# Kernel tuning notes

Hardware: AMD Instinct MI355X
Metric: run time of the kernel (lower is better)

Reference implementation:

```python
import jax, jax.numpy as jnp
import numpy as np

TEMP = 1.0
EPS = 1e-8
NUM_SP = 2048


def setup_inputs() -> dict:
    key = jax.random.key(0)
    k1, k2, k3, k4 = jax.random.split(key, 4)
    N, C, H, W = 8, 19, 512, 512
    inputs = jax.random.normal(k1, (N, C, H, W), dtype=jnp.float32)
    # multi-hot superpixel targets in {0,1}, last column is an extra slot sliced off
    targets = jax.random.randint(k2, (N, NUM_SP, C + 1), 0, 2).astype(jnp.float32)
    superpixels = jax.random.randint(k3, (N, H, W), 0, NUM_SP, dtype=jnp.int32)
    spmasks = jax.random.bernoulli(k4, 0.5, (N, H, W))
    return {"inputs": inputs, "targets": targets,
            "superpixels": superpixels, "spmasks": spmasks}


def reference(inputs, targets, superpixels, spmasks):
    N, C, H, W = inputs.shape
    # N x HW x C, softmax over classes (permute(0,2,3,1).reshape(N,-1,C))
    logits = inputs.reshape(N, C, H * W).transpose(0, 2, 1) / TEMP
    out = jax.nn.softmax(logits, axis=2)                       # N x HW x C
    sp = superpixels.reshape(N, -1)                            # N x HW
    mask = spmasks.reshape(N, -1)                              # N x HW
    trg_sup = jax.lax.stop_gradient(targets[..., :-1])         # N x S x C (detached)
    # gather per-pixel target rows via superpixel index
    trg_pixel = jnp.take_along_axis(trg_sup, sp[:, :, None], axis=1)  # N x HW x C
    # valid = spmask AND target row non-empty
    valid = mask & jnp.any(trg_pixel != 0, axis=2)             # N x HW
    pos_pred = jnp.sum(out * trg_pixel, axis=2)                # N x HW
    loss = -jnp.sum(jnp.where(valid, jnp.log(pos_pred + EPS), 0.0))
    num_valid = 1 + jnp.sum(valid)
    return loss / num_valid
```

## Files before the change

### kernel.cpp

```cpp
#include <hip/hip_runtime.h>

#define HW_   (512 * 512)
#define NIMG  8
#define NC    19
#define NSP   2048
#define TC    20
#define NROWS (NIMG * NSP)
#define NBLK  256
#define NGRP  16
#define GSIZE (NBLK / NGRP)

typedef float vf4 __attribute__((ext_vector_type(4)));
typedef int   vi4 __attribute__((ext_vector_type(4)));


__global__ __launch_bounds__(256) void prep(
    const float* __restrict__ tgt,
    const unsigned int* __restrict__ spm,
    unsigned int* __restrict__ flag, unsigned int* __restrict__ st,
    unsigned int* __restrict__ gt, unsigned int* __restrict__ bm) {

    int gid = blockIdx.x * 256 + threadIdx.x;
    if (gid == 0) *st = 0u;
    if (gid < NGRP) gt[gid * 16] = 0u;

    if (blockIdx.x == 1 && threadIdx.x < 64) {
        unsigned int nonlow = 0, upper = 0;
        for (int i = threadIdx.x; i < 1024; i += 64) {
            unsigned int v = spm[i];
            nonlow |= (v & 0xFEFEFEFEu);
            upper  |= (v & 0xFFFFFF00u);
        }
        unsigned long long b1 = __ballot(nonlow != 0);
        unsigned long long b2 = __ballot(upper != 0);
        if (threadIdx.x == 0)
            *flag = ((b1 == 0ull) && (b2 != 0ull)) ? 0u : 1u;
    }

    const float* row = tgt + (size_t)gid * TC;
    unsigned int m = 0;
#pragma unroll
    for (int c = 0; c < NC; ++c)
        m |= (row[c] != 0.0f ? 1u : 0u) << c;
    bm[gid] = m;
}

__global__ __launch_bounds__(256, 1) void mcce_main(
    const float* __restrict__ x,
    const int*   __restrict__ sp,
    const void*  __restrict__ spm,
    const unsigned int* __restrict__ bmt,
    const unsigned int* __restrict__ flag,
    float* __restrict__ pl, unsigned int* __restrict__ pc,
    unsigned int* __restrict__ st, unsigned int* __restrict__ gt,
    float* __restrict__ out) {

    __shared__ unsigned int bmtab[NSP];
    __shared__ float sL[4];
    __shared__ unsigned int sC[4];

    int b    = blockIdx.x;
    int t    = threadIdx.x;
    int wave = t >> 6;
    int lane = t & 63;

    int n     = b & 7;
    int sbase = (b >> 3) * 8192;
    int wbase = sbase + wave * 2048;
    unsigned int flagv = *flag;

    const vi4* btv = (const vi4*)(bmt + (size_t)n * NSP);
    ((vi4*)bmtab)[t]       = btv[t];
    ((vi4*)bmtab)[t + 256] = btv[t + 256];

    const int* spw = sp + (size_t)n * HW_ + wbase;
    vi4 s4[8];
#pragma unroll
    for (int k = 0; k < 8; ++k)
        s4[k] = ((const vi4*)spw)[lane + k * 64];

    int mkb[8];
    size_t mbase = (size_t)n * HW_ + wbase;
    if (flagv) {
#pragma unroll
        for (int k = 0; k < 8; ++k) {
            vi4 m = ((const vi4*)((const int*)spm + mbase))[lane + k * 64];
            mkb[k] = (m.x != 0 ? 1 : 0) | (m.y != 0 ? 2 : 0) |
                     (m.z != 0 ? 4 : 0) | (m.w != 0 ? 8 : 0);
        }
    } else {
#pragma unroll
        for (int k = 0; k < 8; ++k) {
            unsigned int mw = ((const unsigned int*)
                               ((const unsigned char*)spm + mbase))[lane + k * 64];
            mkb[k] = ((mw        & 0xFFu) ? 1 : 0) | (((mw >> 8)  & 0xFFu) ? 2 : 0) |
                     (((mw >> 16) & 0xFFu) ? 4 : 0) | (((mw >> 24) & 0xFFu) ? 8 : 0);
        }
    }

    __syncthreads();

    unsigned int bv[8][4];
#pragma unroll
    for (int k = 0; k < 8; ++k) {
        bv[k][0] = bmtab[s4[k].x]; bv[k][1] = bmtab[s4[k].y];
        bv[k][2] = bmtab[s4[k].z]; bv[k][3] = bmtab[s4[k].w];
    }

    const float* xw = x + (size_t)n * NC * HW_ + wbase;
    vf4 A[8], B[8];
    vf4 se[8], ts[8];
#pragma unroll
    for (int k = 0; k < 8; ++k) { se[k] = (vf4){0,0,0,0}; ts[k] = (vf4){0,0,0,0}; }

#define LDC(R, c) { const vf4* p_ = (const vf4*)(xw + (size_t)(c) * HW_);      \
    _Pragma("unroll") for (int k_ = 0; k_ < 8; ++k_) R[k_] = p_[lane + k_*64]; }

#define PRC(R, c) { _Pragma("unroll") for (int k_ = 0; k_ < 8; ++k_) {         \
    vf4 e_;                                                                    \
    e_.x = __expf(R[k_].x); e_.y = __expf(R[k_].y);                            \
    e_.z = __expf(R[k_].z); e_.w = __expf(R[k_].w);                            \
    se[k_].x += e_.x; se[k_].y += e_.y; se[k_].z += e_.z; se[k_].w += e_.w;    \
    ts[k_].x += ((bv[k_][0] >> (c)) & 1) ? e_.x : 0.0f;                        \
    ts[k_].y += ((bv[k_][1] >> (c)) & 1) ? e_.y : 0.0f;                        \
    ts[k_].z += ((bv[k_][2] >> (c)) & 1) ? e_.z : 0.0f;                        \
    ts[k_].w += ((bv[k_][3] >> (c)) & 1) ? e_.w : 0.0f; } }

    LDC(A, 0)
#pragma unroll
    for (int p = 0; p < 9; ++p) {
        LDC(B, 2 * p + 1)
        PRC(A, 2 * p)
        LDC(A, 2 * p + 2)
        PRC(B, 2 * p + 1)
    }
    PRC(A, 18)

#undef LDC
#undef PRC

    float lsum = 0.0f;
    unsigned int lcnt = 0;
#pragma unroll
    for (int k = 0; k < 8; ++k) {
        if ((mkb[k] & 1) && bv[k][0]) { lsum -= __logf(ts[k].x / se[k].x + 1e-8f); ++lcnt; }
        if ((mkb[k] & 2) && bv[k][1]) { lsum -= __logf(ts[k].y / se[k].y + 1e-8f); ++lcnt; }
        if ((mkb[k] & 4) && bv[k][2]) { lsum -= __logf(ts[k].z / se[k].z + 1e-8f); ++lcnt; }
        if ((mkb[k] & 8) && bv[k][3]) { lsum -= __logf(ts[k].w / se[k].w + 1e-8f); ++lcnt; }
    }

    for (int o = 32; o > 0; o >>= 1) {
        lsum += __shfl_down(lsum, o);
        lcnt += __shfl_down(lcnt, o);
    }
    __syncthreads();
    if ((t & 63) == 0) { sL[wave] = lsum; sC[wave] = lcnt; }
    __syncthreads();

    if (t == 0) {
        float        L = sL[0] + sL[1] + sL[2] + sL[3];
        unsigned int C = sC[0] + sC[1] + sC[2] + sC[3];
        __hip_atomic_store(&pl[b], L, __ATOMIC_RELAXED, __HIP_MEMORY_SCOPE_AGENT);
        __hip_atomic_store(&pc[b], C, __ATOMIC_RELAXED, __HIP_MEMORY_SCOPE_AGENT);
        unsigned int g = (unsigned int)b / GSIZE;
        unsigned int isLast = 0u;
        unsigned int tk = __hip_atomic_fetch_add(&gt[g * 16], 1u,
                              __ATOMIC_ACQ_REL, __HIP_MEMORY_SCOPE_AGENT);
        if (tk == (unsigned int)(GSIZE - 1)) {
            unsigned int s = __hip_atomic_fetch_add(st, 1u,
                                 __ATOMIC_ACQ_REL, __HIP_MEMORY_SCOPE_AGENT);
            isLast = (s == NGRP - 1) ? 1u : 0u;
        }
        sC[0] = isLast;
    }
    __syncthreads();

    if (sC[0]) {
        float        L = 0.0f;
        unsigned int C = 0u;
        for (int i = t; i < NBLK; i += 256) {
            L += __hip_atomic_load(&pl[i], __ATOMIC_RELAXED, __HIP_MEMORY_SCOPE_AGENT);
            C += __hip_atomic_load(&pc[i], __ATOMIC_RELAXED, __HIP_MEMORY_SCOPE_AGENT);
        }
        for (int o = 32; o > 0; o >>= 1) {
            L += __shfl_down(L, o);
            C += __shfl_down(C, o);
        }
        __syncthreads();
        if ((t & 63) == 0) { sL[wave] = L; sC[wave] = C; }
        __syncthreads();
        if (t == 0) {
            L = sL[0] + sL[1] + sL[2] + sL[3];
            C = sC[0] + sC[1] + sC[2] + sC[3];
            out[0] = L / (float)(1u + C);
        }
    }
}

extern "C" void kernel_launch(void* const* d_in, const int* in_sizes, int n_in,
                              void* d_out, int out_size, void* d_ws, size_t ws_size,
                              hipStream_t stream) {
    const float* x   = (const float*)d_in[0];
    const float* tgt = (const float*)d_in[1];
    const int*   sp  = (const int*)d_in[2];
    const void*  spm = d_in[3];

    unsigned int* flag = (unsigned int*)d_ws;
    unsigned int* st   = (unsigned int*)((char*)d_ws + 4);
    unsigned int* gt   = (unsigned int*)((char*)d_ws + 64);
    float*        pl   = (float*)((char*)d_ws + 1088);
    unsigned int* pc   = (unsigned int*)((char*)d_ws + 3136);
    unsigned int* bmt  = (unsigned int*)((char*)d_ws + 5184);

    prep<<<NROWS / 256, 256, 0, stream>>>(tgt, (const unsigned int*)spm,
                                          flag, st, gt, bmt);

    mcce_main<<<NBLK, 256, 0, stream>>>(x, sp, spm, bmt, flag,
                                        pl, pc, st, gt, (float*)d_out);
}
```

Baseline: 285.2 us.

## Restructure main kernel into per-pixel-tile loop over images with asm double-buffered loads

Each block now owns a 1024-pixel tile and loops over all 8 images. Each thread loads 4 pixels across all 19 channels in one batch of inline-asm nontemporal dwordx4 loads, while the next image's batch is issued before computing the current one. The per-block LDS superpixel bitmask table is dropped in favour of direct global gathers into the bitmask array, which removes the LDS staging and one barrier. It uses far more VGPRs (two 19-vector buffers) and hand-placed vmcnt waits, which risks occupancy limits and fragile ordering.

```diff
diff --git a/kernel.cpp b/kernel.cpp
--- a/kernel.cpp
+++ b/kernel.cpp
@@ -6,6 +6,7 @@
 #define NSP   2048
 #define TC    20
 #define NROWS (NIMG * NSP)
+#define TILE  1024
 #define NBLK  256
 #define NGRP  16
 #define GSIZE (NBLK / NGRP)
@@ -55,113 +56,211 @@
     unsigned int* __restrict__ st, unsigned int* __restrict__ gt,
     float* __restrict__ out) {
 
-    __shared__ unsigned int bmtab[NSP];
     __shared__ float sL[4];
     __shared__ unsigned int sC[4];
 
     int b    = blockIdx.x;
     int t    = threadIdx.x;
     int wave = t >> 6;
-    int lane = t & 63;
-
-    int n     = b & 7;
-    int sbase = (b >> 3) * 8192;
-    int wbase = sbase + wave * 2048;
     unsigned int flagv = *flag;
 
-    const vi4* btv = (const vi4*)(bmt + (size_t)n * NSP);
-    ((vi4*)bmtab)[t]       = btv[t];
-    ((vi4*)bmtab)[t + 256] = btv[t + 256];
-
-    const int* spw = sp + (size_t)n * HW_ + wbase;
-    vi4 s4[8];
-#pragma unroll
-    for (int k = 0; k < 8; ++k)
-        s4[k] = ((const vi4*)spw)[lane + k * 64];
-
-    int mkb[8];
-    size_t mbase = (size_t)n * HW_ + wbase;
-    if (flagv) {
-#pragma unroll
-        for (int k = 0; k < 8; ++k) {
-            vi4 m = ((const vi4*)((const int*)spm + mbase))[lane + k * 64];
-            mkb[k] = (m.x != 0 ? 1 : 0) | (m.y != 0 ? 2 : 0) |
-                     (m.z != 0 ? 4 : 0) | (m.w != 0 ? 8 : 0);
-        }
-    } else {
-#pragma unroll
-        for (int k = 0; k < 8; ++k) {
-            unsigned int mw = ((const unsigned int*)
-                               ((const unsigned char*)spm + mbase))[lane + k * 64];
-            mkb[k] = ((mw        & 0xFFu) ? 1 : 0) | (((mw >> 8)  & 0xFFu) ? 2 : 0) |
-                     (((mw >> 16) & 0xFFu) ? 4 : 0) | (((mw >> 24) & 0xFFu) ? 8 : 0);
-        }
-    }
-
-    __syncthreads();
-
-    unsigned int bv[8][4];
-#pragma unroll
-    for (int k = 0; k < 8; ++k) {
-        bv[k][0] = bmtab[s4[k].x]; bv[k][1] = bmtab[s4[k].y];
-        bv[k][2] = bmtab[s4[k].z]; bv[k][3] = bmtab[s4[k].w];
-    }
-
-    const float* xw = x + (size_t)n * NC * HW_ + wbase;
-    vf4 A[8], B[8];
-    vf4 se[8], ts[8];
-#pragma unroll
-    for (int k = 0; k < 8; ++k) { se[k] = (vf4){0,0,0,0}; ts[k] = (vf4){0,0,0,0}; }
-
-#define LDC(R, c) { const vf4* p_ = (const vf4*)(xw + (size_t)(c) * HW_);      \
-    _Pragma("unroll") for (int k_ = 0; k_ < 8; ++k_) R[k_] = p_[lane + k_*64]; }
-
-#define PRC(R, c) { _Pragma("unroll") for (int k_ = 0; k_ < 8; ++k_) {         \
-    vf4 e_;                                                                    \
-    e_.x = __expf(R[k_].x); e_.y = __expf(R[k_].y);                            \
-    e_.z = __expf(R[k_].z); e_.w = __expf(R[k_].w);                            \
-    se[k_].x += e_.x; se[k_].y += e_.y; se[k_].z += e_.z; se[k_].w += e_.w;    \
-    ts[k_].x += ((bv[k_][0] >> (c)) & 1) ? e_.x : 0.0f;                        \
-    ts[k_].y += ((bv[k_][1] >> (c)) & 1) ? e_.y : 0.0f;                        \
-    ts[k_].z += ((bv[k_][2] >> (c)) & 1) ? e_.z : 0.0f;                        \
-    ts[k_].w += ((bv[k_][3] >> (c)) & 1) ? e_.w : 0.0f; } }
-
-    LDC(A, 0)
-#pragma unroll
-    for (int p = 0; p < 9; ++p) {
-        LDC(B, 2 * p + 1)
-        PRC(A, 2 * p)
-        LDC(A, 2 * p + 2)
-        PRC(B, 2 * p + 1)
-    }
-    PRC(A, 18)
-
-#undef LDC
-#undef PRC
-
+    int tpb = (b & 255) * TILE;
+    size_t thr4 = (size_t)tpb + 4 * t;
+
+    vf4 A[NC], B[NC];
+    vi4 s4A, s4B;
     float lsum = 0.0f;
     unsigned int lcnt = 0;
-#pragma unroll
-    for (int k = 0; k < 8; ++k) {
-        if ((mkb[k] & 1) && bv[k][0]) { lsum -= __logf(ts[k].x / se[k].x + 1e-8f); ++lcnt; }
-        if ((mkb[k] & 2) && bv[k][1]) { lsum -= __logf(ts[k].y / se[k].y + 1e-8f); ++lcnt; }
-        if ((mkb[k] & 4) && bv[k][2]) { lsum -= __logf(ts[k].z / se[k].z + 1e-8f); ++lcnt; }
-        if ((mkb[k] & 8) && bv[k][3]) { lsum -= __logf(ts[k].w / se[k].w + 1e-8f); ++lcnt; }
-    }
+
+#define ISSUE(S4, D, N_) do {                                                  \
+    const float* xb_  = x  + (size_t)(N_) * NC * HW_ + tpb;                    \
+    const int*   spb_ = sp + (size_t)(N_) * HW_ + tpb;                         \
+    unsigned int vo_  = (unsigned int)(t * 16);                                \
+    asm volatile(                                                              \
+        "global_load_dwordx4 %[s4],  %[vo], %[spb]\n\t"                        \
+        "global_load_dwordx4 %[d0],  %[vo], %[xb] nt\n\t"                      \
+        "v_add_u32 %[vo], 0x100000, %[vo]\n\t"                                 \
+        "global_load_dwordx4 %[d1],  %[vo], %[xb] nt\n\t"                      \
+        "v_add_u32 %[vo], 0x100000, %[vo]\n\t"                                 \
+        "global_load_dwordx4 %[d2],  %[vo], %[xb] nt\n\t"                      \
+        "v_add_u32 %[vo], 0x100000, %[vo]\n\t"                                 \
+        "global_load_dwordx4 %[d3],  %[vo], %[xb] nt\n\t"                      \
+        "v_add_u32 %[vo], 0x100000, %[vo]\n\t"                                 \
+        "global_load_dwordx4 %[d4],  %[vo], %[xb] nt\n\t"                      \
+        "v_add_u32 %[vo], 0x100000, %[vo]\n\t"                                 \
+        "global_load_dwordx4 %[d5],  %[vo], %[xb] nt\n\t"                      \
+        "v_add_u32 %[vo], 0x100000, %[vo]\n\t"                                 \
+        "global_load_dwordx4 %[d6],  %[vo], %[xb] nt\n\t"                      \
+        "v_add_u32 %[vo], 0x100000, %[vo]\n\t"                                 \
+        "global_load_dwordx4 %[d7],  %[vo], %[xb] nt\n\t"                      \
+        "v_add_u32 %[vo], 0x100000, %[vo]\n\t"                                 \
+        "global_load_dwordx4 %[d8],  %[vo], %[xb] nt\n\t"                      \
+        "v_add_u32 %[vo], 0x100000, %[vo]\n\t"                                 \
+        "global_load_dwordx4 %[d9],  %[vo], %[xb] nt\n\t"                      \
+        "v_add_u32 %[vo], 0x100000, %[vo]\n\t"                                 \
+        "global_load_dwordx4 %[d10], %[vo], %[xb] nt\n\t"                      \
+        "v_add_u32 %[vo], 0x100000, %[vo]\n\t"                                 \
+        "global_load_dwordx4 %[d11], %[vo], %[xb] nt\n\t"                      \
+        "v_add_u32 %[vo], 0x100000, %[vo]\n\t"                                 \
+        "global_load_dwordx4 %[d12], %[vo], %[xb] nt\n\t"                      \
+        "v_add_u32 %[vo], 0x100000, %[vo]\n\t"                                 \
+        "global_load_dwordx4 %[d13], %[vo], %[xb] nt\n\t"                      \
+        "v_add_u32 %[vo], 0x100000, %[vo]\n\t"                                 \
+        "global_load_dwordx4 %[d14], %[vo], %[xb] nt\n\t"                      \
+        "v_add_u32 %[vo], 0x100000, %[vo]\n\t"                                 \
+        "global_load_dwordx4 %[d15], %[vo], %[xb] nt\n\t"                      \
+        "v_add_u32 %[vo], 0x100000, %[vo]\n\t"                                 \
+        "global_load_dwordx4 %[d16], %[vo], %[xb] nt\n\t"                      \
+        "v_add_u32 %[vo], 0x100000, %[vo]\n\t"                                 \
+        "global_load_dwordx4 %[d17], %[vo], %[xb] nt\n\t"                      \
+        "v_add_u32 %[vo], 0x100000, %[vo]\n\t"                                 \
+        "global_load_dwordx4 %[d18], %[vo], %[xb] nt"                          \
+        : [d0]"=v"(D[0]),  [d1]"=v"(D[1]),  [d2]"=v"(D[2]),  [d3]"=v"(D[3]),   \
+          [d4]"=v"(D[4]),  [d5]"=v"(D[5]),  [d6]"=v"(D[6]),  [d7]"=v"(D[7]),   \
+          [d8]"=v"(D[8]),  [d9]"=v"(D[9]),  [d10]"=v"(D[10]),[d11]"=v"(D[11]), \
+          [d12]"=v"(D[12]),[d13]"=v"(D[13]),[d14]"=v"(D[14]),[d15]"=v"(D[15]), \
+          [d16]"=v"(D[16]),[d17]"=v"(D[17]),[d18]"=v"(D[18]),                  \
+          [s4]"=v"(S4), [vo]"+v"(vo_)                                          \
+        : [xb]"s"(xb_), [spb]"s"(spb_));                                       \
+} while (0)
+
+#define TIES(D) "+v"(D[0]), "+v"(D[1]), "+v"(D[2]), "+v"(D[3]), "+v"(D[4]),    \
+                "+v"(D[5]), "+v"(D[6]), "+v"(D[7]), "+v"(D[8]), "+v"(D[9]),    \
+                "+v"(D[10]), "+v"(D[11]), "+v"(D[12]), "+v"(D[13]),            \
+                "+v"(D[14]), "+v"(D[15]), "+v"(D[16]), "+v"(D[17]), "+v"(D[18])
+
+#define GATH(CS4, IT) \
+    asm volatile("s_waitcnt vmcnt(19)" : "+v"(CS4));                           \
+    __builtin_amdgcn_sched_barrier(0);                                         \
+    const unsigned int* bt_ = bmt + (IT) * NSP;                                \
+    const unsigned int* a0_ = bt_ + CS4.x;                                     \
+    const unsigned int* a1_ = bt_ + CS4.y;                                     \
+    const unsigned int* a2_ = bt_ + CS4.z;                                     \
+    const unsigned int* a3_ = bt_ + CS4.w;                                     \
+    unsigned int g0_, g1_, g2_, g3_;                                           \
+    asm volatile("global_load_dword %0, %4, off\n\t"                           \
+                 "global_load_dword %1, %5, off\n\t"                           \
+                 "global_load_dword %2, %6, off\n\t"                           \
+                 "global_load_dword %3, %7, off"                               \
+        : "=&v"(g0_), "=&v"(g1_), "=&v"(g2_), "=&v"(g3_)                       \
+        : "v"(a0_), "v"(a1_), "v"(a2_), "v"(a3_));
+
+#define COMP(CD) \
+    float se0=0, se1=0, se2=0, se3=0, ts0=0, ts1=0, ts2=0, ts3=0;              \
+    _Pragma("unroll")                                                          \
+    for (int c = 0; c < NC; ++c) {                                             \
+        float e0 = __expf(CD[c].x), e1 = __expf(CD[c].y);                      \
+        float e2 = __expf(CD[c].z), e3 = __expf(CD[c].w);                      \
+        se0 += e0; se1 += e1; se2 += e2; se3 += e3;                            \
+        ts0 += ((g0_ >> c) & 1) ? e0 : 0.0f;                                   \
+        ts1 += ((g1_ >> c) & 1) ? e1 : 0.0f;                                   \
+        ts2 += ((g2_ >> c) & 1) ? e2 : 0.0f;                                   \
+        ts3 += ((g3_ >> c) & 1) ? e3 : 0.0f;                                   \
+    }                                                                          \
+    if ((mk0 != 0) && (g0_ != 0u)) { lsum -= __logf(ts0/se0 + 1e-8f); ++lcnt; }\
+    if ((mk1 != 0) && (g1_ != 0u)) { lsum -= __logf(ts1/se1 + 1e-8f); ++lcnt; }\
+    if ((mk2 != 0) && (g2_ != 0u)) { lsum -= __logf(ts2/se2 + 1e-8f); ++lcnt; }\
+    if ((mk3 != 0) && (g3_ != 0u)) { lsum -= __logf(ts3/se3 + 1e-8f); ++lcnt; }
+
+#define BODY4(CS4, CD, NS4, ND, IT) do {                                       \
+    GATH(CS4, IT)                                                              \
+    vi4 m4_;                                                                   \
+    const vi4* pm_ = (const vi4*)((const int*)spm + (size_t)(IT) * HW_ + thr4);\
+    asm volatile("global_load_dwordx4 %0, %1, off" : "=&v"(m4_) : "v"(pm_));   \
+    ISSUE(NS4, ND, (IT) + 1);                                                  \
+    asm volatile("s_waitcnt vmcnt(20)"                                         \
+        : TIES(CD), "+v"(g0_), "+v"(g1_), "+v"(g2_), "+v"(g3_), "+v"(m4_));    \
+    __builtin_amdgcn_sched_barrier(0);                                         \
+    int mk0 = m4_.x, mk1 = m4_.y, mk2 = m4_.z, mk3 = m4_.w;                    \
+    COMP(CD)                                                                   \
+} while (0)
+
+#define BODY4L(CS4, CD, IT) do {                                               \
+    GATH(CS4, IT)                                                              \
+    vi4 m4_;                                                                   \
+    const vi4* pm_ = (const vi4*)((const int*)spm + (size_t)(IT) * HW_ + thr4);\
+    asm volatile("global_load_dwordx4 %0, %1, off" : "=&v"(m4_) : "v"(pm_));   \
+    asm volatile("s_waitcnt vmcnt(0)"                                          \
+        : TIES(CD), "+v"(g0_), "+v"(g1_), "+v"(g2_), "+v"(g3_), "+v"(m4_));    \
+    __builtin_amdgcn_sched_barrier(0);                                         \
+    int mk0 = m4_.x, mk1 = m4_.y, mk2 = m4_.z, mk3 = m4_.w;                    \
+    COMP(CD)                                                                   \
+} while (0)
+
+#define BODY1(CS4, CD, NS4, ND, IT) do {                                       \
+    GATH(CS4, IT)                                                              \
+    unsigned int mw_;                                                          \
+    const unsigned int* pm_ = (const unsigned int*)                            \
+        ((const unsigned char*)spm + (size_t)(IT) * HW_ + thr4);               \
+    asm volatile("global_load_dword %0, %1, off" : "=&v"(mw_) : "v"(pm_));     \
+    ISSUE(NS4, ND, (IT) + 1);                                                  \
+    asm volatile("s_waitcnt vmcnt(20)"                                         \
+        : TIES(CD), "+v"(g0_), "+v"(g1_), "+v"(g2_), "+v"(g3_), "+v"(mw_));    \
+    __builtin_amdgcn_sched_barrier(0);                                         \
+    int mk0 = mw_ & 0xFF, mk1 = (mw_ >> 8) & 0xFF;                             \
+    int mk2 = (mw_ >> 16) & 0xFF, mk3 = (mw_ >> 24) & 0xFF;                    \
+    COMP(CD)                                                                   \
+} while (0)
+
+#define BODY1L(CS4, CD, IT) do {                                               \
+    GATH(CS4, IT)                                                              \
+    unsigned int mw_;                                                          \
+    const unsigned int* pm_ = (const unsigned int*)                            \
+        ((const unsigned char*)spm + (size_t)(IT) * HW_ + thr4);               \
+    asm volatile("global_load_dword %0, %1, off" : "=&v"(mw_) : "v"(pm_));     \
+    asm volatile("s_waitcnt vmcnt(0)"                                          \
+        : TIES(CD), "+v"(g0_), "+v"(g1_), "+v"(g2_), "+v"(g3_), "+v"(mw_));    \
+    __builtin_amdgcn_sched_barrier(0);                                         \
+    int mk0 = mw_ & 0xFF, mk1 = (mw_ >> 8) & 0xFF;                             \
+    int mk2 = (mw_ >> 16) & 0xFF, mk3 = (mw_ >> 24) & 0xFF;                    \
+    COMP(CD)                                                                   \
+} while (0)
+
+    if (flagv) {
+        ISSUE(s4A, A, 0);
+        BODY4(s4A, A, s4B, B, 0);
+        BODY4(s4B, B, s4A, A, 1);
+        BODY4(s4A, A, s4B, B, 2);
+        BODY4(s4B, B, s4A, A, 3);
+        BODY4(s4A, A, s4B, B, 4);
+        BODY4(s4B, B, s4A, A, 5);
+        BODY4(s4A, A, s4B, B, 6);
+        BODY4L(s4B, B, 7);
+    } else {
+        ISSUE(s4A, A, 0);
+        BODY1(s4A, A, s4B, B, 0);
+        BODY1(s4B, B, s4A, A, 1);
+        BODY1(s4A, A, s4B, B, 2);
+        BODY1(s4B, B, s4A, A, 3);
+        BODY1(s4A, A, s4B, B, 4);
+        BODY1(s4B, B, s4A, A, 5);
+        BODY1(s4A, A, s4B, B, 6);
+        BODY1L(s4B, B, 7);
+    }
+
+#undef BODY1L
+#undef BODY1
+#undef BODY4L
+#undef BODY4
+#undef COMP
+#undef GATH
+#undef TIES
+#undef ISSUE
 
     for (int o = 32; o > 0; o >>= 1) {
         lsum += __shfl_down(lsum, o);
         lcnt += __shfl_down(lcnt, o);
     }
-    __syncthreads();
     if ((t & 63) == 0) { sL[wave] = lsum; sC[wave] = lcnt; }
     __syncthreads();
 
     if (t == 0) {
         float        L = sL[0] + sL[1] + sL[2] + sL[3];
         unsigned int C = sC[0] + sC[1] + sC[2] + sC[3];
-        __hip_atomic_store(&pl[b], L, __ATOMIC_RELAXED, __HIP_MEMORY_SCOPE_AGENT);
-        __hip_atomic_store(&pc[b], C, __ATOMIC_RELAXED, __HIP_MEMORY_SCOPE_AGENT);
+        __hip_atomic_store(&pl[b], L, __ATOMIC_RELAXED,
+                           __HIP_MEMORY_SCOPE_AGENT);
+        __hip_atomic_store(&pc[b], C, __ATOMIC_RELAXED,
+                           __HIP_MEMORY_SCOPE_AGENT);
         unsigned int g = (unsigned int)b / GSIZE;
         unsigned int isLast = 0u;
         unsigned int tk = __hip_atomic_fetch_add(&gt[g * 16], 1u,
@@ -179,8 +278,10 @@
         float        L = 0.0f;
         unsigned int C = 0u;
         for (int i = t; i < NBLK; i += 256) {
-            L += __hip_atomic_load(&pl[i], __ATOMIC_RELAXED, __HIP_MEMORY_SCOPE_AGENT);
-            C += __hip_atomic_load(&pc[i], __ATOMIC_RELAXED, __HIP_MEMORY_SCOPE_AGENT);
+            L += __hip_atomic_load(&pl[i], __ATOMIC_RELAXED,
+                                   __HIP_MEMORY_SCOPE_AGENT);
+            C += __hip_atomic_load(&pc[i], __ATOMIC_RELAXED,
+                                   __HIP_MEMORY_SCOPE_AGENT);
         }
         for (int o = 32; o > 0; o >>= 1) {
             L += __shfl_down(L, o);
```

Result: faster. 231.7 us (-18.8%).
